# Performance work log

Hardware: AMD Instinct MI355X
Metric: run time of the kernel (lower is better)

The kernel has to match this reference:

```python
import jax, jax.numpy as jnp
import numpy as np

D_MODEL, D_K, D_V, H = 1024, 64, 64, 16
B, NQ, NK = 2, 2048, 2048


def setup_inputs() -> dict:
    key = jax.random.key(0)
    ks = jax.random.split(key, 12)
    hd = H * D_K
    xav = lambda k, shape: jax.random.uniform(k, shape, jnp.float32, -1.0, 1.0) * np.sqrt(6.0 / (shape[0] + shape[1]))
    return {
        "queries": jax.random.normal(ks[0], (B, NQ, D_MODEL), jnp.float32),
        "keys": jax.random.normal(ks[1], (B, NK, D_MODEL), jnp.float32),
        "values": jax.random.normal(ks[2], (B, NK, D_MODEL), jnp.float32),
        "memory": jax.random.uniform(ks[3], (B, NK), jnp.float32),
        "Wq": xav(ks[4], (D_MODEL, hd)), "bq": jnp.zeros((hd,), jnp.float32),
        "Wk": xav(ks[5], (D_MODEL, hd)), "bk": jnp.zeros((hd,), jnp.float32),
        "Wv": xav(ks[6], (D_MODEL, H * D_V)), "bv": jnp.zeros((H * D_V,), jnp.float32),
        "Wo": xav(ks[7], (H * D_V, D_MODEL)), "bo": jnp.zeros((D_MODEL,), jnp.float32),
        "Wmm": xav(ks[8], (1, H * D_V)), "bmm": jnp.zeros((H * D_V,), jnp.float32),
    }


def reference(queries, keys, values, memory, Wq, bq, Wk, bk, Wv, bv, Wo, bo, Wmm, bmm):
    b, nq = queries.shape[:2]
    nk = keys.shape[1]
    # projections -> (b, h, n, d)
    q = (queries @ Wq + bq).reshape(b, nq, H, D_K).transpose(0, 2, 1, 3)
    k = (keys @ Wk + bk).reshape(b, nk, H, D_K).transpose(0, 2, 1, 3)
    v = (values @ Wv + bv).reshape(b, nk, H, D_V).transpose(0, 2, 1, 3)
    # memory gate: fc_mm(memory[..., None]) -> (b, nk, h*d_k) -> (b, h, nk, d_k)
    mm = (memory[:, :, None] * Wmm[0] + bmm).reshape(b, nk, H, D_K).transpose(0, 2, 1, 3)
    att = jnp.einsum("bhqd,bhkd->bhqk", q, k * mm) / np.sqrt(D_K).astype(np.float32)
    att = jax.nn.softmax(att, axis=-1)
    out = jnp.einsum("bhqk,bhkd->bhqd", att, v * mm)
    out = out.transpose(0, 2, 1, 3).reshape(b, nq, H * D_V)
    return out @ Wo + bo
```

## Files before the change

### kernel.cpp

```cpp
#include <hip/hip_runtime.h>
#include <hip/hip_bf16.h>

#define H_   16
#define NQ_  2048
#define NK_  2048
#define DM_  1024

typedef float f32x4 __attribute__((ext_vector_type(4)));
typedef float f32x16 __attribute__((ext_vector_type(16)));
typedef __bf16 bf16x8 __attribute__((ext_vector_type(8)));
typedef unsigned short u16x8 __attribute__((ext_vector_type(8)));
typedef unsigned short u16x4 __attribute__((ext_vector_type(4)));

__device__ __forceinline__ unsigned short bfbits(float x) {
  __bf16 h = (__bf16)x;
  return __builtin_bit_cast(unsigned short, h);
}

__global__ __launch_bounds__(256) void cvt3(const float* __restrict__ q,
                                            const float* __restrict__ k,
                                            const float* __restrict__ v,
                                            unsigned short* __restrict__ qo,
                                            unsigned short* __restrict__ ko,
                                            unsigned short* __restrict__ vo) {
  const float* src = (blockIdx.y == 0) ? q : (blockIdx.y == 1) ? k : v;
  unsigned short* dst = (blockIdx.y == 0) ? qo : (blockIdx.y == 1) ? ko : vo;
  int i = blockIdx.x * 256 + threadIdx.x;
  const float4* s4 = (const float4*)src;
  float4 a = s4[2 * i], b = s4[2 * i + 1];
  bf16x8 o;
  o[0] = (__bf16)a.x; o[1] = (__bf16)a.y; o[2] = (__bf16)a.z; o[3] = (__bf16)a.w;
  o[4] = (__bf16)b.x; o[5] = (__bf16)b.y; o[6] = (__bf16)b.z; o[7] = (__bf16)b.w;
  *((bf16x8*)dst + i) = o;
}

__global__ __launch_bounds__(256) void transpose_cvt4(
    const float* __restrict__ s0, const float* __restrict__ s1,
    const float* __restrict__ s2, const float* __restrict__ s3,
    unsigned short* __restrict__ d0, unsigned short* __restrict__ d1,
    unsigned short* __restrict__ d2, unsigned short* __restrict__ d3) {
  const float* src = (blockIdx.z == 0) ? s0 : (blockIdx.z == 1) ? s1 : (blockIdx.z == 2) ? s2 : s3;
  unsigned short* dst = (blockIdx.z == 0) ? d0 : (blockIdx.z == 1) ? d1 : (blockIdx.z == 2) ? d2 : d3;
  __shared__ float t[64][65];
  const int r0 = blockIdx.x * 64, c0 = blockIdx.y * 64;
  for (int i = threadIdx.x; i < 4096; i += 256) {
    int r = i >> 6, c = i & 63;
    t[r][c] = src[(size_t)(r0 + r) * DM_ + c0 + c];
  }
  __syncthreads();
  for (int i = threadIdx.x; i < 4096; i += 256) {
    int n = i >> 6, k = i & 63;
    dst[(size_t)(c0 + n) * DM_ + r0 + k] = bfbits(t[k][n]);
  }
}

__device__ __forceinline__ void gll16(const unsigned short* g, unsigned short* l) {
  __builtin_amdgcn_global_load_lds((const __attribute__((address_space(1))) void*)g,
                                   (__attribute__((address_space(3))) void*)l, 16, 0, 0);
}

template <int MODE>
__device__ __forceinline__ void gemm128_body(
    int bx, int by,
    const unsigned short* __restrict__ A, const unsigned short* __restrict__ Bt, int K,
    const float* __restrict__ bias, const float* __restrict__ mem,
    const float* __restrict__ Wmm, const float* __restrict__ bmm,
    unsigned short* __restrict__ obf,
    unsigned short* Al, unsigned short* Bl) {
  const int tid = threadIdx.x, lane = tid & 63, w = tid >> 6;
  const int wm = w >> 1, wn = w & 1;
  const int m0 = bx * 128, n0 = by * 128;
  const int lrow = lane >> 2, lcol = (lane & 3) * 8;
  const int fr = lane & 15, fk = (lane >> 4) * 8;

  f32x4 acc[4][4] = {};

  const unsigned short* ag0 = A + (size_t)(m0 + w * 32 + lrow) * K + lcol;
  const unsigned short* bg0 = Bt + (size_t)(n0 + w * 32 + lrow) * K + lcol;
  unsigned short* la0 = &Al[(w * 32) * 32];
  unsigned short* la1 = &Al[(w * 32 + 16) * 32];
  unsigned short* lb0 = &Bl[(w * 32) * 32];
  unsigned short* lb1 = &Bl[(w * 32 + 16) * 32];
  const size_t s16K = (size_t)16 * K;

  const int KT = K >> 5;
  for (int kt = 0; kt < KT; ++kt) {
    gll16(ag0, la0); gll16(ag0 + s16K, la1);
    gll16(bg0, lb0); gll16(bg0 + s16K, lb1);
    ag0 += 32; bg0 += 32;
    __syncthreads();
    bf16x8 af[4], bfr[4];
#pragma unroll
    for (int i = 0; i < 4; ++i) af[i] = *(const bf16x8*)&Al[(wm * 64 + i * 16 + fr) * 32 + fk];
#pragma unroll
    for (int j = 0; j < 4; ++j) bfr[j] = *(const bf16x8*)&Bl[(wn * 64 + j * 16 + fr) * 32 + fk];
#pragma unroll
    for (int i = 0; i < 4; ++i)
#pragma unroll
      for (int j = 0; j < 4; ++j)
        acc[i][j] = __builtin_amdgcn_mfma_f32_16x16x32_bf16(af[i], bfr[j], acc[i][j], 0, 0, 0);
    __syncthreads();
  }

#pragma unroll
  for (int i = 0; i < 4; ++i) {
    const int rowb = m0 + wm * 64 + i * 16 + (lane >> 4) * 4;
#pragma unroll
    for (int j = 0; j < 4; ++j) {
      const int col = n0 + wn * 64 + j * 16 + fr;
#pragma unroll
      for (int r = 0; r < 4; ++r) {
        float v = acc[i][j][r];
        int rr = rowb + r;
        if (MODE == 0) {
          int b = rr >> 11, nq = rr & 2047, h = col >> 6, d = col & 63;
          float val = (v + bias[col]) * 0.180336884f;
          obf[(((size_t)(b * H_ + h)) * NQ_ + nq) * 64 + d] = bfbits(val);
        } else if (MODE == 1) {
          int b = rr >> 11, nk = rr & 2047, h = col >> 6, d = col & 63;
          float gate = mem[b * NK_ + nk] * Wmm[col] + bmm[col];
          float val = (v + bias[col]) * gate;
          obf[(((size_t)(b * H_ + h)) * NK_ + nk) * 64 + d] = bfbits(val);
        } else {
          int b = col >> 11, key = col & 2047, h = rr >> 6, d = rr & 63;
          float gate = mem[b * NK_ + key] * Wmm[rr] + bmm[rr];
          float val = (v + bias[rr]) * gate;
          int keyp = (key & ~12) | ((key & 4) << 1) | ((key & 8) >> 1);
          obf[(((size_t)(b * H_ + h)) * 64 + d) * NK_ + keyp] = bfbits(val);
        }
      }
    }
  }
}

__global__ __launch_bounds__(256) void gemm_qkv3(
    const unsigned short* __restrict__ qbf, const unsigned short* __restrict__ kbf,
    const unsigned short* __restrict__ vbf, const unsigned short* __restrict__ WvT,
    const unsigned short* __restrict__ WqT, const unsigned short* __restrict__ WkT,
    const float* __restrict__ bq, const float* __restrict__ bk, const float* __restrict__ bv,
    const float* __restrict__ mem, const float* __restrict__ Wmm, const float* __restrict__ bmm,
    unsigned short* __restrict__ Qp, unsigned short* __restrict__ Kp,
    unsigned short* __restrict__ VpT) {
  __shared__ unsigned short Al[128 * 32];
  __shared__ unsigned short Bl[128 * 32];
  const int gid = (blockIdx.x & 7) * 96 + (blockIdx.x >> 3);
  if (gid < 256) {
    gemm128_body<0>(gid & 31, gid >> 5, qbf, WqT, 1024, bq, nullptr, nullptr, nullptr,
                    Qp, Al, Bl);
  } else if (gid < 512) {
    int bb = gid - 256;
    gemm128_body<1>(bb & 31, bb >> 5, kbf, WkT, 1024, bk, mem, Wmm, bmm, Kp, Al, Bl);
  } else {
    int bb = gid - 512;
    gemm128_body<2>(bb & 7, bb >> 3, WvT, vbf, 1024, bv, mem, Wmm, bmm, VpT, Al, Bl);
  }
}

__global__ __launch_bounds__(256) void gemm_out(
    const unsigned short* __restrict__ AO, const unsigned short* __restrict__ WoT,
    const float* __restrict__ bo, float* __restrict__ out) {
  __shared__ unsigned short Al[64 * 32];
  __shared__ unsigned short Bl[128 * 32];
  const int b = (blockIdx.x & 7) * 64 + (blockIdx.x >> 3);
  const int bx = b & 63, by = b >> 6;
  const int tid = threadIdx.x, lane = tid & 63, w = tid >> 6;
  const int wm = w >> 1, wn = w & 1;
  const int m0 = bx * 64, n0 = by * 128;
  const int lrow = lane >> 2, lcol = (lane & 3) * 8;
  const int fr = lane & 15, fk = (lane >> 4) * 8;
  const int K = 1024;

  f32x4 acc[2][4] = {};

  const unsigned short* ag = AO + (size_t)(m0 + w * 16 + lrow) * K + lcol;
  const unsigned short* bg = WoT + (size_t)(n0 + w * 32 + lrow) * K + lcol;
  unsigned short* la0 = &Al[(w * 16) * 32];
  unsigned short* lb0 = &Bl[(w * 32) * 32];
  unsigned short* lb1 = &Bl[(w * 32 + 16) * 32];
  const size_t s16K = (size_t)16 * K;

  for (int kt = 0; kt < 32; ++kt) {
    gll16(ag, la0);
    gll16(bg, lb0); gll16(bg + s16K, lb1);
    ag += 32; bg += 32;
    __syncthreads();
    bf16x8 af[2], bfr[4];
#pragma unroll
    for (int i = 0; i < 2; ++i) af[i] = *(const bf16x8*)&Al[(wm * 32 + i * 16 + fr) * 32 + fk];
#pragma unroll
    for (int j = 0; j < 4; ++j) bfr[j] = *(const bf16x8*)&Bl[(wn * 64 + j * 16 + fr) * 32 + fk];
#pragma unroll
    for (int i = 0; i < 2; ++i)
#pragma unroll
      for (int j = 0; j < 4; ++j)
        acc[i][j] = __builtin_amdgcn_mfma_f32_16x16x32_bf16(af[i], bfr[j], acc[i][j], 0, 0, 0);
    __syncthreads();
  }

#pragma unroll
  for (int i = 0; i < 2; ++i) {
    const int rowb = m0 + wm * 32 + i * 16 + (lane >> 4) * 4;
#pragma unroll
    for (int j = 0; j < 4; ++j) {
      const int col = n0 + wn * 64 + j * 16 + fr;
#pragma unroll
      for (int r = 0; r < 4; ++r)
        out[(size_t)(rowb + r) * DM_ + col] = acc[i][j][r] + bo[col];
    }
  }
}

__global__ __launch_bounds__(256, 2) void flash_attn(const unsigned short* __restrict__ Qp,
                                                     const unsigned short* __restrict__ Kp,
                                                     const unsigned short* __restrict__ VpT,
                                                     unsigned short* __restrict__ AO) {
  __shared__ unsigned short Ks[2][64][66];
  __shared__ unsigned short Vs[2][64][66];

  const int tid = threadIdx.x, lane = tid & 63, w = tid >> 6;
  const int gid = (blockIdx.x & 7) * 64 + (blockIdx.x >> 3);
  const int bh = gid >> 4;
  const int qt = gid & 15;
  const int r31 = lane & 31, hi2 = lane >> 5;

  const unsigned short* qg = Qp + (((size_t)bh * NQ_) + qt * 128 + w * 32 + r31) * 64 + hi2 * 8;
  bf16x8 qf0 = *(const bf16x8*)&qg[0];
  bf16x8 qf1 = *(const bf16x8*)&qg[16];
  bf16x8 qf2 = *(const bf16x8*)&qg[32];
  bf16x8 qf3 = *(const bf16x8*)&qg[48];

  const int srow = tid >> 2, scol = (tid & 3) * 16;
  const unsigned short* kg = Kp + ((size_t)bh * NK_ + srow) * 64 + scol;
  const unsigned short* vg = VpT + ((size_t)bh * 64 + srow) * NK_ + scol;

  f32x16 acc0 = {}, acc1 = {};
  float m_run = -1e30f, l_run = 0.0f;

  *(u16x8*)&Ks[0][srow][scol]     = *(const u16x8*)(kg);
  *(u16x8*)&Ks[0][srow][scol + 8] = *(const u16x8*)(kg + 8);
  *(u16x8*)&Vs[0][srow][scol]     = *(const u16x8*)(vg);
  *(u16x8*)&Vs[0][srow][scol + 8] = *(const u16x8*)(vg + 8);

  u16x8 kr0, kr1, vr0, vr1;
  for (int kt = 0; kt < 32; ++kt) {
    const int cur = kt & 1;
    if (kt + 1 < 32) {
      const unsigned short* kn = kg + (kt + 1) * 64 * 64;
      const unsigned short* vn = vg + (kt + 1) * 64;
      kr0 = *(const u16x8*)kn; kr1 = *(const u16x8*)(kn + 8);
      vr0 = *(const u16x8*)vn; vr1 = *(const u16x8*)(vn + 8);
    }
    __syncthreads();

    f32x16 sv0 = {}, sv1 = {};
    __builtin_amdgcn_s_setprio(1);
#pragma unroll
    for (int s = 0; s < 4; ++s) {
      bf16x8 qf = (s == 0) ? qf0 : (s == 1) ? qf1 : (s == 2) ? qf2 : qf3;
      bf16x8 ka0 = *(const bf16x8*)&Ks[cur][r31][s * 16 + hi2 * 8];
      bf16x8 ka1 = *(const bf16x8*)&Ks[cur][32 + r31][s * 16 + hi2 * 8];
      sv0 = __builtin_amdgcn_mfma_f32_32x32x16_bf16(ka0, qf, sv0, 0, 0, 0);
      sv1 = __builtin_amdgcn_mfma_f32_32x32x16_bf16(ka1, qf, sv1, 0, 0, 0);
    }
    __builtin_amdgcn_s_setprio(0);

    float mx = fmaxf(sv0[0], sv0[1]);
#pragma unroll
    for (int g = 2; g < 16; ++g) mx = fmaxf(mx, sv0[g]);
#pragma unroll
    for (int g = 0; g < 16; ++g) mx = fmaxf(mx, sv1[g]);
    mx = fmaxf(mx, __shfl_xor(mx, 32));

    if (__any(mx > m_run + 8.0f)) {
      float mnew = fmaxf(m_run, mx);
      float sc = __builtin_amdgcn_exp2f(m_run - mnew);
      m_run = mnew;
      l_run *= sc;
      acc0 *= sc;
      acc1 *= sc;
    }

    float ps = 0.0f;
    bf16x8 pb0, pb1, pb2, pb3;
#pragma unroll
    for (int g = 0; g < 16; ++g) {
      float p0 = __builtin_amdgcn_exp2f(sv0[g] - m_run);
      float p1 = __builtin_amdgcn_exp2f(sv1[g] - m_run);
      ps += p0 + p1;
      if (g < 8) { pb0[g] = (__bf16)p0; pb2[g] = (__bf16)p1; }
      else       { pb1[g - 8] = (__bf16)p0; pb3[g - 8] = (__bf16)p1; }
    }
    ps += __shfl_xor(ps, 32);
    l_run += ps;

    __builtin_amdgcn_s_setprio(1);
#pragma unroll
    for (int t = 0; t < 4; ++t) {
      bf16x8 pb = (t == 0) ? pb0 : (t == 1) ? pb1 : (t == 2) ? pb2 : pb3;
      bf16x8 va0 = *(const bf16x8*)&Vs[cur][r31][t * 16 + hi2 * 8];
      bf16x8 va1 = *(const bf16x8*)&Vs[cur][32 + r31][t * 16 + hi2 * 8];
      acc0 = __builtin_amdgcn_mfma_f32_32x32x16_bf16(va0, pb, acc0, 0, 0, 0);
      acc1 = __builtin_amdgcn_mfma_f32_32x32x16_bf16(va1, pb, acc1, 0, 0, 0);
    }
    __builtin_amdgcn_s_setprio(0);

    if (kt + 1 < 32) {
      *(u16x8*)&Ks[cur ^ 1][srow][scol]     = kr0;
      *(u16x8*)&Ks[cur ^ 1][srow][scol + 8] = kr1;
      *(u16x8*)&Vs[cur ^ 1][srow][scol]     = vr0;
      *(u16x8*)&Vs[cur ^ 1][srow][scol + 8] = vr1;
    }
  }

  const int b = bh >> 4, h = bh & 15;
  const float linv = 1.0f / l_run;
  const int qrow = qt * 128 + w * 32 + r31;
  const size_t rowbase = (((size_t)b * NQ_ + qrow) << 10) + h * 64;
#pragma unroll
  for (int c = 0; c < 4; ++c) {
    u16x4 o0, o1;
#pragma unroll
    for (int i = 0; i < 4; ++i) {
      o0[i] = bfbits(acc0[c * 4 + i] * linv);
      o1[i] = bfbits(acc1[c * 4 + i] * linv);
    }
    *(u16x4*)&AO[rowbase + 8 * c + 4 * hi2]      = o0;
    *(u16x4*)&AO[rowbase + 32 + 8 * c + 4 * hi2] = o1;
  }
}

extern "C" void kernel_launch(void* const* d_in, const int* in_sizes, int n_in,
                              void* d_out, int out_size, void* d_ws, size_t ws_size,
                              hipStream_t stream) {
  const float* queries = (const float*)d_in[0];
  const float* keys    = (const float*)d_in[1];
  const float* values  = (const float*)d_in[2];
  const float* memory  = (const float*)d_in[3];
  const float* Wq  = (const float*)d_in[4];
  const float* bq  = (const float*)d_in[5];
  const float* Wk  = (const float*)d_in[6];
  const float* bk  = (const float*)d_in[7];
  const float* Wv  = (const float*)d_in[8];
  const float* bv  = (const float*)d_in[9];
  const float* Wo  = (const float*)d_in[10];
  const float* bo  = (const float*)d_in[11];
  const float* Wmm = (const float*)d_in[12];
  const float* bmm = (const float*)d_in[13];

  char* ws = (char*)d_ws;
  const size_t SZ_X = (size_t)4096 * 1024 * 2;
  const size_t SZ_W = (size_t)1024 * 1024 * 2;
  unsigned short* qbf = (unsigned short*)(ws);
  unsigned short* kbf = (unsigned short*)(ws + SZ_X);
  unsigned short* vbf = (unsigned short*)(ws + 2 * SZ_X);
  unsigned short* AO  = (unsigned short*)(ws);
  size_t off = 3 * SZ_X;
  unsigned short* WqT = (unsigned short*)(ws + off); off += SZ_W;
  unsigned short* WkT = (unsigned short*)(ws + off); off += SZ_W;
  unsigned short* WvT = (unsigned short*)(ws + off); off += SZ_W;
  unsigned short* WoT = (unsigned short*)(ws + off); off += SZ_W;
  unsigned short* Qp  = (unsigned short*)(ws + off); off += SZ_X;
  unsigned short* Kp  = (unsigned short*)(ws + off); off += SZ_X;
  unsigned short* VpT = (unsigned short*)(ws + off); off += SZ_X;

  cvt3<<<dim3(2048, 3), 256, 0, stream>>>(queries, keys, values, qbf, kbf, vbf);
  transpose_cvt4<<<dim3(16, 16, 4), 256, 0, stream>>>(Wq, Wk, Wv, Wo, WqT, WkT, WvT, WoT);

  gemm_qkv3<<<768, 256, 0, stream>>>(qbf, kbf, vbf, WvT, WqT, WkT,
                                     bq, bk, bv, memory, Wmm, bmm, Qp, Kp, VpT);

  flash_attn<<<512, 256, 0, stream>>>(Qp, Kp, VpT, AO);

  gemm_out<<<512, 256, 0, stream>>>(AO, WoT, bo, (float*)d_out);
}
```

Before: 138.1 us.

## Double flash-attention key tile to 128 and merge prep kernels into one launch

```diff
diff --git a/kernel.cpp b/kernel.cpp
--- a/kernel.cpp
+++ b/kernel.cpp
@@ -17,40 +17,42 @@
   return __builtin_bit_cast(unsigned short, h);
 }
 
-__global__ __launch_bounds__(256) void cvt3(const float* __restrict__ q,
-                                            const float* __restrict__ k,
-                                            const float* __restrict__ v,
-                                            unsigned short* __restrict__ qo,
-                                            unsigned short* __restrict__ ko,
-                                            unsigned short* __restrict__ vo) {
-  const float* src = (blockIdx.y == 0) ? q : (blockIdx.y == 1) ? k : v;
-  unsigned short* dst = (blockIdx.y == 0) ? qo : (blockIdx.y == 1) ? ko : vo;
-  int i = blockIdx.x * 256 + threadIdx.x;
-  const float4* s4 = (const float4*)src;
-  float4 a = s4[2 * i], b = s4[2 * i + 1];
-  bf16x8 o;
-  o[0] = (__bf16)a.x; o[1] = (__bf16)a.y; o[2] = (__bf16)a.z; o[3] = (__bf16)a.w;
-  o[4] = (__bf16)b.x; o[5] = (__bf16)b.y; o[6] = (__bf16)b.z; o[7] = (__bf16)b.w;
-  *((bf16x8*)dst + i) = o;
-}
-
-__global__ __launch_bounds__(256) void transpose_cvt4(
-    const float* __restrict__ s0, const float* __restrict__ s1,
-    const float* __restrict__ s2, const float* __restrict__ s3,
-    unsigned short* __restrict__ d0, unsigned short* __restrict__ d1,
-    unsigned short* __restrict__ d2, unsigned short* __restrict__ d3) {
-  const float* src = (blockIdx.z == 0) ? s0 : (blockIdx.z == 1) ? s1 : (blockIdx.z == 2) ? s2 : s3;
-  unsigned short* dst = (blockIdx.z == 0) ? d0 : (blockIdx.z == 1) ? d1 : (blockIdx.z == 2) ? d2 : d3;
+__global__ __launch_bounds__(256) void prep(
+    const float* __restrict__ Wq, const float* __restrict__ Wk,
+    const float* __restrict__ Wv, const float* __restrict__ Wo,
+    unsigned short* __restrict__ WqT, unsigned short* __restrict__ WkT,
+    unsigned short* __restrict__ WvT, unsigned short* __restrict__ WoT,
+    const float* __restrict__ q, const float* __restrict__ k, const float* __restrict__ v,
+    unsigned short* __restrict__ qo, unsigned short* __restrict__ ko,
+    unsigned short* __restrict__ vo) {
   __shared__ float t[64][65];
-  const int r0 = blockIdx.x * 64, c0 = blockIdx.y * 64;
-  for (int i = threadIdx.x; i < 4096; i += 256) {
-    int r = i >> 6, c = i & 63;
-    t[r][c] = src[(size_t)(r0 + r) * DM_ + c0 + c];
-  }
-  __syncthreads();
-  for (int i = threadIdx.x; i < 4096; i += 256) {
-    int n = i >> 6, k = i & 63;
-    dst[(size_t)(c0 + n) * DM_ + r0 + k] = bfbits(t[k][n]);
+  const int flat = blockIdx.x;
+  if (flat < 1024) {
+    const int z = flat >> 8, bx = (flat >> 4) & 15, by = flat & 15;
+    const float* src = (z == 0) ? Wq : (z == 1) ? Wk : (z == 2) ? Wv : Wo;
+    unsigned short* dst = (z == 0) ? WqT : (z == 1) ? WkT : (z == 2) ? WvT : WoT;
+    const int r0 = bx * 64, c0 = by * 64;
+    for (int i = threadIdx.x; i < 4096; i += 256) {
+      int r = i >> 6, c = i & 63;
+      t[r][c] = src[(size_t)(r0 + r) * DM_ + c0 + c];
+    }
+    __syncthreads();
+    for (int i = threadIdx.x; i < 4096; i += 256) {
+      int n = i >> 6, kk = i & 63;
+      dst[(size_t)(c0 + n) * DM_ + r0 + kk] = bfbits(t[kk][n]);
+    }
+  } else {
+    const int tt = flat - 1024;
+    const int which = tt >> 11;
+    const float* src = (which == 0) ? q : (which == 1) ? k : v;
+    unsigned short* dst = (which == 0) ? qo : (which == 1) ? ko : vo;
+    const int i = (tt & 2047) * 256 + threadIdx.x;
+    const float4* s4 = (const float4*)src;
+    float4 a = s4[2 * i], b = s4[2 * i + 1];
+    bf16x8 o;
+    o[0] = (__bf16)a.x; o[1] = (__bf16)a.y; o[2] = (__bf16)a.z; o[3] = (__bf16)a.w;
+    o[4] = (__bf16)b.x; o[5] = (__bf16)b.y; o[6] = (__bf16)b.z; o[7] = (__bf16)b.w;
+    *((bf16x8*)dst + i) = o;
   }
 }
 
@@ -214,8 +216,8 @@
                                                      const unsigned short* __restrict__ Kp,
                                                      const unsigned short* __restrict__ VpT,
                                                      unsigned short* __restrict__ AO) {
-  __shared__ unsigned short Ks[2][64][66];
-  __shared__ unsigned short Vs[2][64][66];
+  __shared__ unsigned short Ks[2][128][66];
+  __shared__ unsigned short Vs[2][64][130];
 
   const int tid = threadIdx.x, lane = tid & 63, w = tid >> 6;
   const int gid = (blockIdx.x & 7) * 64 + (blockIdx.x >> 3);
@@ -224,51 +226,65 @@
   const int r31 = lane & 31, hi2 = lane >> 5;
 
   const unsigned short* qg = Qp + (((size_t)bh * NQ_) + qt * 128 + w * 32 + r31) * 64 + hi2 * 8;
-  bf16x8 qf0 = *(const bf16x8*)&qg[0];
-  bf16x8 qf1 = *(const bf16x8*)&qg[16];
-  bf16x8 qf2 = *(const bf16x8*)&qg[32];
-  bf16x8 qf3 = *(const bf16x8*)&qg[48];
-
-  const int srow = tid >> 2, scol = (tid & 3) * 16;
-  const unsigned short* kg = Kp + ((size_t)bh * NK_ + srow) * 64 + scol;
-  const unsigned short* vg = VpT + ((size_t)bh * 64 + srow) * NK_ + scol;
+  bf16x8 qf[4];
+#pragma unroll
+  for (int s = 0; s < 4; ++s) qf[s] = *(const bf16x8*)&qg[s * 16];
+
+  const int krow = tid >> 1, kcol = (tid & 1) * 32;
+  const int vrow = tid >> 2, vcol = (tid & 3) * 32;
+  const unsigned short* kg = Kp + ((size_t)bh * NK_ + krow) * 64 + kcol;
+  const unsigned short* vg = VpT + ((size_t)bh * 64 + vrow) * NK_ + vcol;
 
   f32x16 acc0 = {}, acc1 = {};
   float m_run = -1e30f, l_run = 0.0f;
 
-  *(u16x8*)&Ks[0][srow][scol]     = *(const u16x8*)(kg);
-  *(u16x8*)&Ks[0][srow][scol + 8] = *(const u16x8*)(kg + 8);
-  *(u16x8*)&Vs[0][srow][scol]     = *(const u16x8*)(vg);
-  *(u16x8*)&Vs[0][srow][scol + 8] = *(const u16x8*)(vg + 8);
-
-  u16x8 kr0, kr1, vr0, vr1;
-  for (int kt = 0; kt < 32; ++kt) {
+  u16x8 kr[4], vr[4];
+#pragma unroll
+  for (int i = 0; i < 4; ++i) {
+    kr[i] = *(const u16x8*)(kg + 8 * i);
+    vr[i] = *(const u16x8*)(vg + 8 * i);
+  }
+#pragma unroll
+  for (int i = 0; i < 4; ++i) {
+    *(u16x8*)&Ks[0][krow][kcol + 8 * i] = kr[i];
+    *(u16x8*)&Vs[0][vrow][vcol + 8 * i] = vr[i];
+  }
+
+  for (int kt = 0; kt < 16; ++kt) {
     const int cur = kt & 1;
-    if (kt + 1 < 32) {
-      const unsigned short* kn = kg + (kt + 1) * 64 * 64;
-      const unsigned short* vn = vg + (kt + 1) * 64;
-      kr0 = *(const u16x8*)kn; kr1 = *(const u16x8*)(kn + 8);
-      vr0 = *(const u16x8*)vn; vr1 = *(const u16x8*)(vn + 8);
-    }
-    __syncthreads();
-
-    f32x16 sv0 = {}, sv1 = {};
+    __syncthreads();
+
+    f32x16 sv[4] = {};
     __builtin_amdgcn_s_setprio(1);
 #pragma unroll
     for (int s = 0; s < 4; ++s) {
-      bf16x8 qf = (s == 0) ? qf0 : (s == 1) ? qf1 : (s == 2) ? qf2 : qf3;
-      bf16x8 ka0 = *(const bf16x8*)&Ks[cur][r31][s * 16 + hi2 * 8];
-      bf16x8 ka1 = *(const bf16x8*)&Ks[cur][32 + r31][s * 16 + hi2 * 8];
-      sv0 = __builtin_amdgcn_mfma_f32_32x32x16_bf16(ka0, qf, sv0, 0, 0, 0);
-      sv1 = __builtin_amdgcn_mfma_f32_32x32x16_bf16(ka1, qf, sv1, 0, 0, 0);
+#pragma unroll
+      for (int kb = 0; kb < 4; ++kb) {
+        bf16x8 ka = *(const bf16x8*)&Ks[cur][kb * 32 + r31][s * 16 + hi2 * 8];
+        sv[kb] = __builtin_amdgcn_mfma_f32_32x32x16_bf16(ka, qf[s], sv[kb], 0, 0, 0);
+      }
     }
     __builtin_amdgcn_s_setprio(0);
 
-    float mx = fmaxf(sv0[0], sv0[1]);
-#pragma unroll
-    for (int g = 2; g < 16; ++g) mx = fmaxf(mx, sv0[g]);
-#pragma unroll
-    for (int g = 0; g < 16; ++g) mx = fmaxf(mx, sv1[g]);
+    if (kt + 1 < 16) {
+      const unsigned short* kn = kg + (size_t)(kt + 1) * 128 * 64;
+      const unsigned short* vn = vg + (kt + 1) * 128;
+#pragma unroll
+      for (int i = 0; i < 4; ++i) {
+        kr[i] = *(const u16x8*)(kn + 8 * i);
+        vr[i] = *(const u16x8*)(vn + 8 * i);
+      }
+    }
+
+    float mxp[4];
+#pragma unroll
+    for (int kb = 0; kb < 4; ++kb) {
+      float m = fmaxf(sv[kb][0], sv[kb][1]);
+#pragma unroll
+      for (int g = 2; g < 16; ++g) m = fmaxf(m, sv[kb][g]);
+      mxp[kb] = m;
+    }
+    float mx = fmaxf(fmaxf(mxp[0], mxp[1]), fmaxf(mxp[2], mxp[3]));
     mx = fmaxf(mx, __shfl_xor(mx, 32));
 
     if (__any(mx > m_run + 8.0f)) {
@@ -280,35 +296,37 @@
       acc1 *= sc;
     }
 
-    float ps = 0.0f;
-    bf16x8 pb0, pb1, pb2, pb3;
-#pragma unroll
-    for (int g = 0; g < 16; ++g) {
-      float p0 = __builtin_amdgcn_exp2f(sv0[g] - m_run);
-      float p1 = __builtin_amdgcn_exp2f(sv1[g] - m_run);
-      ps += p0 + p1;
-      if (g < 8) { pb0[g] = (__bf16)p0; pb2[g] = (__bf16)p1; }
-      else       { pb1[g - 8] = (__bf16)p0; pb3[g - 8] = (__bf16)p1; }
-    }
+    float psp[4] = {0.f, 0.f, 0.f, 0.f};
+    bf16x8 pb[8];
+#pragma unroll
+    for (int kb = 0; kb < 4; ++kb) {
+#pragma unroll
+      for (int g = 0; g < 16; ++g) {
+        float p = __builtin_amdgcn_exp2f(sv[kb][g] - m_run);
+        psp[kb] += p;
+        pb[2 * kb + (g >> 3)][g & 7] = (__bf16)p;
+      }
+    }
+    float ps = (psp[0] + psp[1]) + (psp[2] + psp[3]);
     ps += __shfl_xor(ps, 32);
     l_run += ps;
 
     __builtin_amdgcn_s_setprio(1);
 #pragma unroll
-    for (int t = 0; t < 4; ++t) {
-      bf16x8 pb = (t == 0) ? pb0 : (t == 1) ? pb1 : (t == 2) ? pb2 : pb3;
-      bf16x8 va0 = *(const bf16x8*)&Vs[cur][r31][t * 16 + hi2 * 8];
-      bf16x8 va1 = *(const bf16x8*)&Vs[cur][32 + r31][t * 16 + hi2 * 8];
-      acc0 = __builtin_amdgcn_mfma_f32_32x32x16_bf16(va0, pb, acc0, 0, 0, 0);
-      acc1 = __builtin_amdgcn_mfma_f32_32x32x16_bf16(va1, pb, acc1, 0, 0, 0);
+    for (int ks = 0; ks < 8; ++ks) {
+      bf16x8 va0 = *(const bf16x8*)&Vs[cur][r31][ks * 16 + hi2 * 8];
+      bf16x8 va1 = *(const bf16x8*)&Vs[cur][32 + r31][ks * 16 + hi2 * 8];
+      acc0 = __builtin_amdgcn_mfma_f32_32x32x16_bf16(va0, pb[ks], acc0, 0, 0, 0);
+      acc1 = __builtin_amdgcn_mfma_f32_32x32x16_bf16(va1, pb[ks], acc1, 0, 0, 0);
     }
     __builtin_amdgcn_s_setprio(0);
 
-    if (kt + 1 < 32) {
-      *(u16x8*)&Ks[cur ^ 1][srow][scol]     = kr0;
-      *(u16x8*)&Ks[cur ^ 1][srow][scol + 8] = kr1;
-      *(u16x8*)&Vs[cur ^ 1][srow][scol]     = vr0;
-      *(u16x8*)&Vs[cur ^ 1][srow][scol + 8] = vr1;
+    if (kt + 1 < 16) {
+#pragma unroll
+      for (int i = 0; i < 4; ++i) {
+        *(u16x8*)&Ks[cur ^ 1][krow][kcol + 8 * i] = kr[i];
+        *(u16x8*)&Vs[cur ^ 1][vrow][vcol + 8 * i] = vr[i];
+      }
     }
   }
 
@@ -363,8 +381,8 @@
   unsigned short* Kp  = (unsigned short*)(ws + off); off += SZ_X;
   unsigned short* VpT = (unsigned short*)(ws + off); off += SZ_X;
 
-  cvt3<<<dim3(2048, 3), 256, 0, stream>>>(queries, keys, values, qbf, kbf, vbf);
-  transpose_cvt4<<<dim3(16, 16, 4), 256, 0, stream>>>(Wq, Wk, Wv, Wo, WqT, WkT, WvT, WoT);
+  prep<<<7168, 256, 0, stream>>>(Wq, Wk, Wv, Wo, WqT, WkT, WvT, WoT,
+                                 queries, keys, values, qbf, kbf, vbf);
 
   gemm_qkv3<<<768, 256, 0, stream>>>(qbf, kbf, vbf, WvT, WqT, WkT,
                                      bq, bk, bv, memory, Wmm, bmm, Qp, Kp, VpT);
```

Result: faster. 132.4 us (-4.1%).
